# Performance work log

Measured on AMD Instinct MI355X. Metric: run time of the kernel, lower is better.

Reference implementation:

```python
import jax, jax.numpy as jnp
import numpy as np

N_HEADS = 16

def setup_inputs() -> dict:
    key = jax.random.key(0)
    k1, k2, k3 = jax.random.split(key, 3)
    B, T, C = 2, 2048, 1024
    x = jax.random.normal(k1, (B, T, C), dtype=jnp.float32)
    w_attn = jax.random.normal(k2, (3 * C, C), dtype=jnp.float32) * (C ** -0.5)
    b_attn = jnp.zeros((3 * C,), dtype=jnp.float32)
    w_proj = jax.random.normal(k3, (C, C), dtype=jnp.float32) * (C ** -0.5)
    b_proj = jnp.zeros((C,), dtype=jnp.float32)
    return {"x": x, "w_attn": w_attn, "b_attn": b_attn, "w_proj": w_proj, "b_proj": b_proj}

def reference(x, w_attn, b_attn, w_proj, b_proj):
    B, T, C = x.shape
    H = N_HEADS
    Dh = C // H
    qkv = x @ w_attn.T + b_attn                      # [B,T,3C]
    q, k, v = jnp.split(qkv, 3, axis=-1)             # each [B,T,C]
    q = q.reshape(B, T, H, Dh).transpose(0, 2, 1, 3)  # [B,H,T,Dh]
    k = k.reshape(B, T, H, Dh).transpose(0, 2, 1, 3)
    v = v.reshape(B, T, H, Dh).transpose(0, 2, 1, 3)
    scores = jnp.einsum('bhqd,bhkd->bhqk', q, k) * (Dh ** -0.5)  # [B,H,T,T]
    causal = jnp.tril(jnp.ones((T, T), dtype=bool))
    scores = jnp.where(causal, scores, jnp.float32(-jnp.inf))
    probs = jax.nn.softmax(scores, axis=-1)
    out = jnp.einsum('bhqk,bhkd->bhqd', probs, v)    # [B,H,T,Dh]
    out = out.transpose(0, 2, 1, 3).reshape(B, T, C)
    out = out @ w_proj.T + b_proj
    return out
```

## Files before the change

kernel.cpp:

```cpp
#include <hip/hip_runtime.h>
#include <math.h>

#define GB 2
#define GT_SEQ 2048
#define GC 1024
#define GH 16
#define GDH 64
#define GM (GB * GT_SEQ)

typedef __attribute__((ext_vector_type(8))) short bf16x8;
typedef __attribute__((ext_vector_type(8))) unsigned short u16x8;
typedef __attribute__((ext_vector_type(4))) unsigned short u16x4;
typedef __attribute__((ext_vector_type(4))) float f32x4;
typedef unsigned int u32;

#define QSCALE 0.18033688f

__device__ __forceinline__ unsigned short f2bf(float f) {
    unsigned int u = __float_as_uint(f);
    u += 0x7FFFu + ((u >> 16) & 1u);
    return (unsigned short)(u >> 16);
}
__device__ __forceinline__ float bf2f(unsigned short u) {
    return __uint_as_float(((unsigned int)u) << 16);
}
__device__ __forceinline__ float hw_exp2(float x) {
    return __builtin_amdgcn_exp2f(x);
}
__device__ __forceinline__ u32 pack2bf(float lo, float hi) {
    return ((u32)f2bf(hi) << 16) | (u32)f2bf(lo);
}

#define GLOAD_LDS16(g, l) __builtin_amdgcn_global_load_lds( \
    (const __attribute__((address_space(1))) void*)(g),      \
    (__attribute__((address_space(3))) void*)(l), 16, 0, 0)

__device__ __forceinline__ bf16x8 frag_ld(const char* base, int r, int kch) {
    return *reinterpret_cast<const bf16x8*>(base + r * 128 + ((kch ^ (r & 7)) << 4));
}

__global__ __launch_bounds__(256) void cast3_f32_bf16(
    const float* __restrict__ a, unsigned short* __restrict__ oa, int na,
    const float* __restrict__ b, unsigned short* __restrict__ ob, int nb,
    const float* __restrict__ c, unsigned short* __restrict__ oc)
{
    const int i = (blockIdx.x * 256 + threadIdx.x) * 4;
    const float* src; unsigned short* dst; int off;
    if (i < na)            { src = a; dst = oa; off = i; }
    else if (i < na + nb)  { src = b; dst = ob; off = i - na; }
    else                   { src = c; dst = oc; off = i - na - nb; }
    const float4 v = *reinterpret_cast<const float4*>(&src[off]);
    ushort4 o;
    o.x = f2bf(v.x); o.y = f2bf(v.y); o.z = f2bf(v.z); o.w = f2bf(v.w);
    *reinterpret_cast<ushort4*>(&dst[off]) = o;
}

__global__ __launch_bounds__(256) void gemm_mfma_bt(
    const unsigned short* __restrict__ A,
    const unsigned short* __restrict__ B,
    const float* __restrict__ bias,
    float* __restrict__ Cf,
    unsigned short* __restrict__ Cb,
    int M, int N, int K)
{
    __shared__ char As[128 * 128];
    __shared__ char Bs[128 * 128];

    const int tid  = threadIdx.x;
    const int lane = tid & 63;
    const int w    = tid >> 6;
    const int wm   = w >> 1;
    const int wn   = w & 1;
    const int m0 = blockIdx.y * 128;
    const int n0 = blockIdx.x * 128;

    f32x4 acc[4][4];
#pragma unroll
    for (int i = 0; i < 4; ++i)
#pragma unroll
        for (int j = 0; j < 4; ++j) acc[i][j] = (f32x4){0.f, 0.f, 0.f, 0.f};

    const int wbase = (tid & ~63);

    for (int k0 = 0; k0 < K; k0 += 64) {
        const char* Ag = (const char*)(A + (size_t)m0 * K + k0);
        const char* Bg = (const char*)(B + (size_t)n0 * K + k0);
#pragma unroll
        for (int i = 0; i < 4; ++i) {
            const int c = i * 256 + tid;
            const int row = c >> 3, cin = c & 7;
            const size_t goff = (size_t)row * (K * 2) + (size_t)((cin ^ (row & 7)) << 4);
            GLOAD_LDS16(Ag + goff, As + (i * 256 + wbase) * 16);
            GLOAD_LDS16(Bg + goff, Bs + (i * 256 + wbase) * 16);
        }
        __syncthreads();

#pragma unroll
        for (int ks = 0; ks < 2; ++ks) {
            const int kch = ks * 4 + (lane >> 4);
            bf16x8 a[4], b[4];
#pragma unroll
            for (int mi = 0; mi < 4; ++mi)
                a[mi] = frag_ld(As, wm * 64 + mi * 16 + (lane & 15), kch);
#pragma unroll
            for (int ni = 0; ni < 4; ++ni)
                b[ni] = frag_ld(Bs, wn * 64 + ni * 16 + (lane & 15), kch);
#pragma unroll
            for (int mi = 0; mi < 4; ++mi)
#pragma unroll
                for (int ni = 0; ni < 4; ++ni)
                    acc[mi][ni] = __builtin_amdgcn_mfma_f32_16x16x32_bf16(
                        a[mi], b[ni], acc[mi][ni], 0, 0, 0);
        }
        __syncthreads();
    }

    const int lc  = lane & 15;
    const int lr4 = (lane >> 4) * 4;
#pragma unroll
    for (int ni = 0; ni < 4; ++ni) {
        const int gcol = n0 + wn * 64 + ni * 16 + lc;
        const float bv = bias[gcol];
#pragma unroll
        for (int mi = 0; mi < 4; ++mi) {
            const int grow0 = m0 + wm * 64 + mi * 16 + lr4;
#pragma unroll
            for (int j = 0; j < 4; ++j) {
                const float v = acc[mi][ni][j] + bv;
                if (Cb) Cb[(size_t)(grow0 + j) * N + gcol] = f2bf(v);
                else    Cf[(size_t)(grow0 + j) * N + gcol] = v;
            }
        }
    }
}

__global__ __launch_bounds__(256) void transpose_v(
    const unsigned short* __restrict__ qkvb, unsigned short* __restrict__ Vt)
{
    __shared__ unsigned short vt[64][72];
    const int tid = threadIdx.x;
    const int t0  = blockIdx.x * 64;
    const int bh  = blockIdx.y;
    const int b = bh >> 4, h = bh & 15;
    const unsigned short* src = qkvb + (size_t)(b * GT_SEQ) * (3 * GC) + 2 * GC + h * GDH;
    unsigned short* dstb = Vt + (size_t)bh * GDH * GT_SEQ;

#pragma unroll
    for (int i = 0; i < 2; ++i) {
        const int c = i * 256 + tid;
        const int tr = c >> 3, ch = c & 7;
        *reinterpret_cast<u16x8*>(&vt[tr][ch * 8]) =
            *reinterpret_cast<const u16x8*>(src + (size_t)(t0 + tr) * (3 * GC) + ch * 8);
    }
    __syncthreads();
#pragma unroll
    for (int i = 0; i < 2; ++i) {
        const int c = i * 256 + tid;
        const int d = c >> 3, ch = c & 7;
        u16x8 o;
#pragma unroll
        for (int e = 0; e < 8; ++e) o[e] = vt[ch * 8 + e][d];
        *reinterpret_cast<u16x8*>(dstb + (size_t)d * GT_SEQ + t0 + ch * 8) = o;
    }
}

__global__ __launch_bounds__(256) void flash_attn_mfma8(
    const unsigned short* __restrict__ qkvb,
    const unsigned short* __restrict__ Vt,
    unsigned short* __restrict__ O)
{
    __shared__ __align__(16) char Ks[2][64 * 128];
    __shared__ __align__(16) char Vs[2][64 * 128];

    const int tid  = threadIdx.x;
    const int lane = tid & 63;
    const int w    = tid >> 6;
    const int l15  = lane & 15;
    const int l4   = lane >> 4;
    const int bid  = blockIdx.x;
    const int xcd  = bid & 7;
    const int rest = bid >> 3;
    const int bh   = xcd * 4 + (rest & 3);
    const int qb   = 15 - (rest >> 2);
    const int b    = bh >> 4, h = bh & 15;
    const int q0w  = qb * 128 + w * 32;

    const unsigned short* hQ = qkvb + (size_t)(b * GT_SEQ) * (3 * GC) + h * GDH;
    const char* hKc = (const char*)(qkvb + (size_t)(b * GT_SEQ) * (3 * GC) + GC + h * GDH);
    const char* hVc = (const char*)(Vt + (size_t)bh * GDH * GT_SEQ);

    bf16x8 qf[2][2];
#pragma unroll
    for (int mi = 0; mi < 2; ++mi)
#pragma unroll
        for (int s = 0; s < 2; ++s) {
            bf16x8 v = *reinterpret_cast<const bf16x8*>(
                hQ + (size_t)(q0w + mi * 16 + l15) * (3 * GC) + s * 32 + l4 * 8);
#pragma unroll
            for (int e = 0; e < 8; ++e)
                v[e] = (short)f2bf(bf2f((unsigned short)v[e]) * QSCALE);
            qf[mi][s] = v;
        }

    f32x4 acc_o[2][4];
    float l_part[2];
    float m_r[2];
#pragma unroll
    for (int mi = 0; mi < 2; ++mi) {
        l_part[mi] = 0.f;
        m_r[mi] = -1e30f;
#pragma unroll
        for (int nd = 0; nd < 4; ++nd) acc_o[mi][nd] = (f32x4){0.f, 0.f, 0.f, 0.f};
    }

    const int nt = qb * 2 + 2;
    const int wbase16 = (tid & ~63) * 16;

    auto STAGE = [&](int bb, int t) {
        const int k0 = t * 64;
#pragma unroll
        for (int i = 0; i < 2; ++i) {
            const int c = i * 256 + tid;
            const int row = c >> 3, cin = c & 7;
            GLOAD_LDS16(hKc + (size_t)(k0 + row) * (3 * GC * 2) + ((cin ^ (row & 7)) << 4),
                        Ks[bb] + i * 4096 + wbase16);
            GLOAD_LDS16(hVc + (size_t)row * 4096 + (size_t)k0 * 2 + ((cin ^ (row & 7)) << 4),
                        Vs[bb] + i * 4096 + wbase16);
        }
    };

    STAGE(0, 0);
    __syncthreads();

    for (int t = 0; t < nt; ++t) {
        if (t + 1 < nt) STAGE((t + 1) & 1, t + 1);

        const int k0 = t * 64;
        const char* Kb = Ks[t & 1];
        const char* Vb = Vs[t & 1];

        if (k0 <= q0w + 31) {
            f32x4 s_acc[2][4];
#pragma unroll
            for (int mi = 0; mi < 2; ++mi)
#pragma unroll
                for (int ni = 0; ni < 4; ++ni) s_acc[mi][ni] = (f32x4){0.f, 0.f, 0.f, 0.f};
#pragma unroll
            for (int s = 0; s < 2; ++s) {
                bf16x8 kf[4];
#pragma unroll
                for (int ni = 0; ni < 4; ++ni)
                    kf[ni] = frag_ld(Kb, ni * 16 + l15, s * 4 + l4);
#pragma unroll
                for (int ni = 0; ni < 4; ++ni)
#pragma unroll
                    for (int mi = 0; mi < 2; ++mi)
                        s_acc[mi][ni] = __builtin_amdgcn_mfma_f32_16x16x32_bf16(
                            kf[ni], qf[mi][s], s_acc[mi][ni], 0, 0, 0);
            }

            if (k0 + 63 > q0w) {
#pragma unroll
                for (int mi = 0; mi < 2; ++mi)
#pragma unroll
                    for (int ni = 0; ni < 4; ++ni)
#pragma unroll
                        for (int j = 0; j < 4; ++j)
                            if (k0 + ni * 16 + l4 * 4 + j > q0w + mi * 16 + l15)
                                s_acc[mi][ni][j] = -1e30f;
            }

            float rp[2];
            int ok = 1;
#pragma unroll
            for (int mi = 0; mi < 2; ++mi) {
                float r = fmaxf(fmaxf(s_acc[mi][0][0], s_acc[mi][0][1]),
                                fmaxf(s_acc[mi][0][2], s_acc[mi][0][3]));
#pragma unroll
                for (int ni = 1; ni < 4; ++ni)
                    r = fmaxf(r, fmaxf(fmaxf(s_acc[mi][ni][0], s_acc[mi][ni][1]),
                                       fmaxf(s_acc[mi][ni][2], s_acc[mi][ni][3])));
                rp[mi] = r;
                ok &= (r <= m_r[mi] + 8.f) ? 1 : 0;
            }
            if (!__all(ok)) {
#pragma unroll
                for (int mi = 0; mi < 2; ++mi) {
                    float r = rp[mi];
                    r = fmaxf(r, __shfl_xor(r, 16));
                    r = fmaxf(r, __shfl_xor(r, 32));
                    const float mnew = fmaxf(m_r[mi], r);
                    const float corr = hw_exp2(m_r[mi] - mnew);
                    m_r[mi] = mnew;
                    l_part[mi] *= corr;
#pragma unroll
                    for (int nd = 0; nd < 4; ++nd) acc_o[mi][nd] *= corr;
                }
            }

#pragma unroll
            for (int s = 0; s < 2; ++s) {
                union { u32 w4[4]; bf16x8 v; } pw[2];
#pragma unroll
                for (int mi = 0; mi < 2; ++mi) {
                    f32x4 pa, pb;
#pragma unroll
                    for (int j = 0; j < 4; ++j) {
                        pa[j] = hw_exp2(s_acc[mi][2 * s + 0][j] - m_r[mi]);
                        pb[j] = hw_exp2(s_acc[mi][2 * s + 1][j] - m_r[mi]);
                    }
                    l_part[mi] += (pa[0] + pa[1]) + (pa[2] + pa[3])
                                + (pb[0] + pb[1]) + (pb[2] + pb[3]);
                    pw[mi].w4[0] = pack2bf(pa[0], pa[1]);
                    pw[mi].w4[1] = pack2bf(pa[2], pa[3]);
                    pw[mi].w4[2] = pack2bf(pb[0], pb[1]);
                    pw[mi].w4[3] = pack2bf(pb[2], pb[3]);
                }
                const int ch0 = s * 4 + (l4 >> 1);
                const int sub = (l4 & 1) * 8;
#pragma unroll
                for (int nd = 0; nd < 4; ++nd) {
                    const int d  = nd * 16 + l15;
                    const char* vrow = Vb + d * 128;
                    union { u16x4 h2[2]; bf16x8 v; } vbs;
                    vbs.h2[0] = *reinterpret_cast<const u16x4*>(
                        vrow + ((ch0 ^ (d & 7)) << 4) + sub);
                    vbs.h2[1] = *reinterpret_cast<const u16x4*>(
                        vrow + (((ch0 + 2) ^ (d & 7)) << 4) + sub);
#pragma unroll
                    for (int mi = 0; mi < 2; ++mi)
                        acc_o[mi][nd] = __builtin_amdgcn_mfma_f32_16x16x32_bf16(
                            vbs.v, pw[mi].v, acc_o[mi][nd], 0, 0, 0);
                }
            }
        }

        __syncthreads();
    }

#pragma unroll
    for (int mi = 0; mi < 2; ++mi) {
        float lp = l_part[mi];
        lp += __shfl_xor(lp, 16);
        lp += __shfl_xor(lp, 32);
        const float inv = 1.f / lp;
        const int q = q0w + mi * 16 + l15;
        const size_t rbase = (size_t)(b * GT_SEQ + q) * GC + h * GDH;
#pragma unroll
        for (int nd = 0; nd < 4; ++nd) {
            ushort4 ov;
            ov.x = f2bf(acc_o[mi][nd][0] * inv);
            ov.y = f2bf(acc_o[mi][nd][1] * inv);
            ov.z = f2bf(acc_o[mi][nd][2] * inv);
            ov.w = f2bf(acc_o[mi][nd][3] * inv);
            *reinterpret_cast<ushort4*>(&O[rbase + nd * 16 + l4 * 4]) = ov;
        }
    }
}

extern "C" void kernel_launch(void* const* d_in, const int* in_sizes, int n_in,
                              void* d_out, int out_size, void* d_ws, size_t ws_size,
                              hipStream_t stream) {
    (void)in_sizes; (void)n_in; (void)out_size; (void)ws_size;
    const float* x      = (const float*)d_in[0];
    const float* w_attn = (const float*)d_in[1];
    const float* b_attn = (const float*)d_in[2];
    const float* w_proj = (const float*)d_in[3];
    const float* b_proj = (const float*)d_in[4];
    float* out = (float*)d_out;

    unsigned short* xb   = (unsigned short*)d_ws;
    unsigned short* wab  = xb   + (size_t)GM * GC;
    unsigned short* wpb  = wab  + (size_t)3 * GC * GC;
    unsigned short* qkvb = wpb  + (size_t)GC * GC;
    unsigned short* Vt   = qkvb + (size_t)GM * 3 * GC;
    unsigned short* aob  = xb;

    cast3_f32_bf16<<<dim3(8192), dim3(256), 0, stream>>>(
        x, xb, GM * GC, w_attn, wab, 3 * GC * GC, w_proj, wpb);

    gemm_mfma_bt<<<dim3(3 * GC / 128, GM / 128), dim3(256), 0, stream>>>(
        xb, wab, b_attn, nullptr, qkvb, GM, 3 * GC, GC);

    transpose_v<<<dim3(GT_SEQ / 64, GB * GH), dim3(256), 0, stream>>>(qkvb, Vt);

    flash_attn_mfma8<<<dim3(512), dim3(256), 0, stream>>>(qkvb, Vt, aob);

    gemm_mfma_bt<<<dim3(GC / 128, GM / 128), dim3(256), 0, stream>>>(
        aob, wpb, b_proj, out, nullptr, GM, GC, GC);
}
```

Baseline: 121.9 us.

## Retile flash attention to 64-row blocks, fold Q scale into GEMM, swizzle GEMM blocks

Splits attention into 1024 two-wave workgroups of 64 query rows instead of 512 four-wave groups, giving finer causal load balancing and more resident blocks. The Q scaling moves into the QKV GEMM epilogue, and the GEMM gains an XCD-aware block swizzle for cache locality. V is pre-permuted in the transpose so fragments load with a single 16-byte LDS read. The softmax row sum is computed by an MFMA against a ones vector, and packing uses the library bf16x2 conversion. The smaller workgroups may lose some K/V reuse per staged tile.

```diff
diff --git a/kernel.cpp b/kernel.cpp
--- a/kernel.cpp
+++ b/kernel.cpp
@@ -1,4 +1,5 @@
 #include <hip/hip_runtime.h>
+#include <hip/hip_bf16.h>
 #include <math.h>
 
 #define GB 2
@@ -10,7 +11,6 @@
 
 typedef __attribute__((ext_vector_type(8))) short bf16x8;
 typedef __attribute__((ext_vector_type(8))) unsigned short u16x8;
-typedef __attribute__((ext_vector_type(4))) unsigned short u16x4;
 typedef __attribute__((ext_vector_type(4))) float f32x4;
 typedef unsigned int u32;
 
@@ -27,8 +27,9 @@
 __device__ __forceinline__ float hw_exp2(float x) {
     return __builtin_amdgcn_exp2f(x);
 }
-__device__ __forceinline__ u32 pack2bf(float lo, float hi) {
-    return ((u32)f2bf(hi) << 16) | (u32)f2bf(lo);
+__device__ __forceinline__ u32 pk_bf16(float lo, float hi) {
+    __hip_bfloat162 h = __float22bfloat162_rn(make_float2(lo, hi));
+    return *reinterpret_cast<u32*>(&h);
 }
 
 #define GLOAD_LDS16(g, l) __builtin_amdgcn_global_load_lds( \
@@ -71,8 +72,14 @@
     const int w    = tid >> 6;
     const int wm   = w >> 1;
     const int wn   = w & 1;
-    const int m0 = blockIdx.y * 128;
-    const int n0 = blockIdx.x * 128;
+
+    const int gx  = gridDim.x;
+    const int lid = blockIdx.y * gx + blockIdx.x;
+    const int nwg = gx * gridDim.y;
+    const int cpx = nwg >> 3;
+    const int swz = (lid & 7) * cpx + (lid >> 3);
+    const int m0 = (swz / gx) * 128;
+    const int n0 = (swz % gx) * 128;
 
     f32x4 acc[4][4];
 #pragma unroll
@@ -121,12 +128,13 @@
     for (int ni = 0; ni < 4; ++ni) {
         const int gcol = n0 + wn * 64 + ni * 16 + lc;
         const float bv = bias[gcol];
+        const float scl = (Cb && gcol < GC) ? QSCALE : 1.f;
 #pragma unroll
         for (int mi = 0; mi < 4; ++mi) {
             const int grow0 = m0 + wm * 64 + mi * 16 + lr4;
 #pragma unroll
             for (int j = 0; j < 4; ++j) {
-                const float v = acc[mi][ni][j] + bv;
+                const float v = (acc[mi][ni][j] + bv) * scl;
                 if (Cb) Cb[(size_t)(grow0 + j) * N + gcol] = f2bf(v);
                 else    Cf[(size_t)(grow0 + j) * N + gcol] = v;
             }
@@ -157,14 +165,18 @@
     for (int i = 0; i < 2; ++i) {
         const int c = i * 256 + tid;
         const int d = c >> 3, ch = c & 7;
+        const int s = ch >> 2, l4p = ch & 3;
         u16x8 o;
 #pragma unroll
-        for (int e = 0; e < 8; ++e) o[e] = vt[ch * 8 + e][d];
+        for (int e = 0; e < 8; ++e) {
+            const int tp = s * 32 + (e >> 2) * 16 + l4p * 4 + (e & 3);
+            o[e] = vt[tp][d];
+        }
         *reinterpret_cast<u16x8*>(dstb + (size_t)d * GT_SEQ + t0 + ch * 8) = o;
     }
 }
 
-__global__ __launch_bounds__(256) void flash_attn_mfma8(
+__global__ __launch_bounds__(128) void flash_attn_mfma10(
     const unsigned short* __restrict__ qkvb,
     const unsigned short* __restrict__ Vt,
     unsigned short* __restrict__ O)
@@ -181,51 +193,50 @@
     const int xcd  = bid & 7;
     const int rest = bid >> 3;
     const int bh   = xcd * 4 + (rest & 3);
-    const int qb   = 15 - (rest >> 2);
+    const int qb   = 31 - (rest >> 2);
     const int b    = bh >> 4, h = bh & 15;
-    const int q0w  = qb * 128 + w * 32;
+    const int q0w  = qb * 64 + w * 32;
 
     const unsigned short* hQ = qkvb + (size_t)(b * GT_SEQ) * (3 * GC) + h * GDH;
     const char* hKc = (const char*)(qkvb + (size_t)(b * GT_SEQ) * (3 * GC) + GC + h * GDH);
     const char* hVc = (const char*)(Vt + (size_t)bh * GDH * GT_SEQ);
 
+    bf16x8 ones_a;
+#pragma unroll
+    for (int e = 0; e < 8; ++e) ones_a[e] = (short)0x3F80;
+
     bf16x8 qf[2][2];
 #pragma unroll
     for (int mi = 0; mi < 2; ++mi)
 #pragma unroll
-        for (int s = 0; s < 2; ++s) {
-            bf16x8 v = *reinterpret_cast<const bf16x8*>(
+        for (int s = 0; s < 2; ++s)
+            qf[mi][s] = *reinterpret_cast<const bf16x8*>(
                 hQ + (size_t)(q0w + mi * 16 + l15) * (3 * GC) + s * 32 + l4 * 8);
-#pragma unroll
-            for (int e = 0; e < 8; ++e)
-                v[e] = (short)f2bf(bf2f((unsigned short)v[e]) * QSCALE);
-            qf[mi][s] = v;
-        }
 
     f32x4 acc_o[2][4];
-    float l_part[2];
+    f32x4 acc_l[2];
     float m_r[2];
 #pragma unroll
     for (int mi = 0; mi < 2; ++mi) {
-        l_part[mi] = 0.f;
+        acc_l[mi] = (f32x4){0.f, 0.f, 0.f, 0.f};
         m_r[mi] = -1e30f;
 #pragma unroll
         for (int nd = 0; nd < 4; ++nd) acc_o[mi][nd] = (f32x4){0.f, 0.f, 0.f, 0.f};
     }
 
-    const int nt = qb * 2 + 2;
+    const int nt = qb + 1;
     const int wbase16 = (tid & ~63) * 16;
 
     auto STAGE = [&](int bb, int t) {
         const int k0 = t * 64;
 #pragma unroll
-        for (int i = 0; i < 2; ++i) {
-            const int c = i * 256 + tid;
+        for (int i = 0; i < 4; ++i) {
+            const int c = i * 128 + tid;
             const int row = c >> 3, cin = c & 7;
             GLOAD_LDS16(hKc + (size_t)(k0 + row) * (3 * GC * 2) + ((cin ^ (row & 7)) << 4),
-                        Ks[bb] + i * 4096 + wbase16);
+                        Ks[bb] + i * 2048 + wbase16);
             GLOAD_LDS16(hVc + (size_t)row * 4096 + (size_t)k0 * 2 + ((cin ^ (row & 7)) << 4),
-                        Vs[bb] + i * 4096 + wbase16);
+                        Vs[bb] + i * 2048 + wbase16);
         }
     };
 
@@ -244,7 +255,8 @@
 #pragma unroll
             for (int mi = 0; mi < 2; ++mi)
 #pragma unroll
-                for (int ni = 0; ni < 4; ++ni) s_acc[mi][ni] = (f32x4){0.f, 0.f, 0.f, 0.f};
+                for (int ni = 0; ni < 4; ++ni)
+                    s_acc[mi][ni] = (f32x4){0.f, 0.f, 0.f, 0.f};
 #pragma unroll
             for (int s = 0; s < 2; ++s) {
                 bf16x8 kf[4];
@@ -292,7 +304,7 @@
                     const float mnew = fmaxf(m_r[mi], r);
                     const float corr = hw_exp2(m_r[mi] - mnew);
                     m_r[mi] = mnew;
-                    l_part[mi] *= corr;
+                    acc_l[mi] *= corr;
 #pragma unroll
                     for (int nd = 0; nd < 4; ++nd) acc_o[mi][nd] *= corr;
                 }
@@ -309,28 +321,20 @@
                         pa[j] = hw_exp2(s_acc[mi][2 * s + 0][j] - m_r[mi]);
                         pb[j] = hw_exp2(s_acc[mi][2 * s + 1][j] - m_r[mi]);
                     }
-                    l_part[mi] += (pa[0] + pa[1]) + (pa[2] + pa[3])
-                                + (pb[0] + pb[1]) + (pb[2] + pb[3]);
-                    pw[mi].w4[0] = pack2bf(pa[0], pa[1]);
-                    pw[mi].w4[1] = pack2bf(pa[2], pa[3]);
-                    pw[mi].w4[2] = pack2bf(pb[0], pb[1]);
-                    pw[mi].w4[3] = pack2bf(pb[2], pb[3]);
+                    pw[mi].w4[0] = pk_bf16(pa[0], pa[1]);
+                    pw[mi].w4[1] = pk_bf16(pa[2], pa[3]);
+                    pw[mi].w4[2] = pk_bf16(pb[0], pb[1]);
+                    pw[mi].w4[3] = pk_bf16(pb[2], pb[3]);
+                    acc_l[mi] = __builtin_amdgcn_mfma_f32_16x16x32_bf16(
+                        ones_a, pw[mi].v, acc_l[mi], 0, 0, 0);
                 }
-                const int ch0 = s * 4 + (l4 >> 1);
-                const int sub = (l4 & 1) * 8;
 #pragma unroll
                 for (int nd = 0; nd < 4; ++nd) {
-                    const int d  = nd * 16 + l15;
-                    const char* vrow = Vb + d * 128;
-                    union { u16x4 h2[2]; bf16x8 v; } vbs;
-                    vbs.h2[0] = *reinterpret_cast<const u16x4*>(
-                        vrow + ((ch0 ^ (d & 7)) << 4) + sub);
-                    vbs.h2[1] = *reinterpret_cast<const u16x4*>(
-                        vrow + (((ch0 + 2) ^ (d & 7)) << 4) + sub);
+                    const bf16x8 vf = frag_ld(Vb, nd * 16 + l15, s * 4 + l4);
 #pragma unroll
                     for (int mi = 0; mi < 2; ++mi)
                         acc_o[mi][nd] = __builtin_amdgcn_mfma_f32_16x16x32_bf16(
-                            vbs.v, pw[mi].v, acc_o[mi][nd], 0, 0, 0);
+                            vf, pw[mi].v, acc_o[mi][nd], 0, 0, 0);
                 }
             }
         }
@@ -340,10 +344,7 @@
 
 #pragma unroll
     for (int mi = 0; mi < 2; ++mi) {
-        float lp = l_part[mi];
-        lp += __shfl_xor(lp, 16);
-        lp += __shfl_xor(lp, 32);
-        const float inv = 1.f / lp;
+        const float inv = 1.f / acc_l[mi][0];
         const int q = q0w + mi * 16 + l15;
         const size_t rbase = (size_t)(b * GT_SEQ + q) * GC + h * GDH;
 #pragma unroll
@@ -384,7 +385,7 @@
 
     transpose_v<<<dim3(GT_SEQ / 64, GB * GH), dim3(256), 0, stream>>>(qkvb, Vt);
 
-    flash_attn_mfma8<<<dim3(512), dim3(256), 0, stream>>>(qkvb, Vt, aob);
+    flash_attn_mfma10<<<dim3(1024), dim3(128), 0, stream>>>(qkvb, Vt, aob);
 
     gemm_mfma_bt<<<dim3(GC / 128, GM / 128), dim3(256), 0, stream>>>(
         aob, wpb, b_proj, out, nullptr, GM, GC, GC);
```

Measured after the change: 125.2 us. 1.03x slower.
